# Performance work log

Measured on AMD Instinct MI355X. Metric: run time of the kernel, lower is better.

The kernel has to match this reference:

```python
import jax, jax.numpy as jnp
import numpy as np

N_NODES = 100000
N_EDGES = 1600000
N_GRAPHS = 512


def gcn_conv(x, row, col, W, b):
    # x: [N, Cin], row/col: [E] (self-loops already appended)
    n = x.shape[0]
    h = x @ W                                        # [N, Cout]
    deg = jax.ops.segment_sum(jnp.ones_like(col, dtype=x.dtype), col, num_segments=n)
    dinv = jnp.where(deg > 0, deg ** -0.5, 0.0)
    norm = dinv[row] * dinv[col]                     # [E]
    msg = norm[:, None] * h[row]                     # [E, Cout]
    out = jax.ops.segment_sum(msg, col, num_segments=n)
    return out + b


def setup_inputs() -> dict:
    key = jax.random.key(0)
    ks = jax.random.split(key, 10)
    x = jax.random.normal(ks[0], (N_NODES, 128), dtype=jnp.float32)
    edge_index = jax.random.randint(ks[1], (2, N_EDGES), 0, N_NODES, dtype=jnp.int64)
    batch = jnp.sort(jax.random.randint(ks[2], (N_NODES,), 0, N_GRAPHS, dtype=jnp.int64))
    def lin_w(k, fan_in, fan_out):
        bound = 1.0 / np.sqrt(fan_in)
        return jax.random.uniform(k, (fan_in, fan_out), jnp.float32, -bound, bound)
    # GCN layers (bias zero-initialized per reset_parameters)
    W1 = lin_w(ks[3], 128, 128); b1 = jnp.zeros((128,), jnp.float32)
    W2 = lin_w(ks[4], 128, 128); b2 = jnp.zeros((128,), jnp.float32)
    # MLP layers (Linear with bias)
    Wm1 = lin_w(ks[5], 128, 64)
    bm1 = jax.random.uniform(ks[6], (64,), jnp.float32, -1/np.sqrt(128), 1/np.sqrt(128))
    Wm2 = lin_w(ks[7], 64, 1)
    bm2 = jax.random.uniform(ks[8], (1,), jnp.float32, -1/np.sqrt(64), 1/np.sqrt(64))
    return {"x": x, "edge_index": edge_index, "batch": batch,
            "W1": W1, "b1": b1, "W2": W2, "b2": b2,
            "Wm1": Wm1, "bm1": bm1, "Wm2": Wm2, "bm2": bm2}


def reference(x, edge_index, batch, W1, b1, W2, b2, Wm1, bm1, Wm2, bm2):
    n = x.shape[0]
    loops = jnp.arange(n, dtype=edge_index.dtype)
    row = jnp.concatenate([edge_index[0], loops])
    col = jnp.concatenate([edge_index[1], loops])
    # GCN: conv -> relu -> conv
    h = gcn_conv(x, row, col, W1, b1)
    h = jax.nn.relu(h)
    h = gcn_conv(h, row, col, W2, b2)
    # scatter-mean pooling over graphs
    sums = jax.ops.segment_sum(h, batch, num_segments=N_GRAPHS)      # [G, C]
    counts = jax.ops.segment_sum(jnp.ones((n,), h.dtype), batch, num_segments=N_GRAPHS)
    g = sums / jnp.maximum(counts, 1.0)[:, None]
    # MLP: linear -> relu -> linear
    g = jax.nn.relu(g @ Wm1 + bm1)
    out = g @ Wm2 + bm2
    return out
```

## Files before the change

kernel.cpp:

```cpp
#include <hip/hip_runtime.h>
#include <math.h>

#define C_DIM 128
#define POOL_CHUNK 64
#define BKT_SHIFT 7
#define MAX_B 1024
#define CB 256
#define CHUNK_MAX 6400
#define FB_CAP 8192
typedef unsigned short ushort_t;
typedef __attribute__((ext_vector_type(8))) short short8;
typedef __attribute__((ext_vector_type(4))) float f32x4;

static inline int ceil_div(int a, int b) { return (a + b - 1) / b; }

__device__ inline ushort_t f2bf(float f) {
    union { float f; unsigned u; } v; v.f = f;
    unsigned r = v.u + 0x7FFFu + ((v.u >> 16) & 1u);
    return (ushort_t)(r >> 16);
}
__device__ inline float bf2f(unsigned s) {
    union { unsigned u; float f; } v; v.u = s << 16; return v.f;
}
__device__ inline float bf_lo(unsigned u) {
    union { unsigned v; float f; } c; c.v = u << 16; return c.f;
}
__device__ inline float bf_hi(unsigned u) {
    union { unsigned v; float f; } c; c.v = u & 0xFFFF0000u; return c.f;
}
__device__ inline void accum8(uint4 u, float acc[8]) {
    acc[0] += bf_lo(u.x); acc[1] += bf_hi(u.x);
    acc[2] += bf_lo(u.y); acc[3] += bf_hi(u.y);
    acc[4] += bf_lo(u.z); acc[5] += bf_hi(u.z);
    acc[6] += bf_lo(u.w); acc[7] += bf_hi(u.w);
}


__global__ __launch_bounds__(256) void k_sortchunk(
    const int* __restrict__ row, const int* __restrict__ col, int E, int chunk,
    int B, int* __restrict__ counts, int* __restrict__ sstart,
    int* __restrict__ epk,
    const float* __restrict__ W1, const float* __restrict__ W2,
    uint4* __restrict__ wf1, uint4* __restrict__ wf2,
    float* __restrict__ gsums, int GC, int* __restrict__ cursor) {
    int t = threadIdx.x, blk = blockIdx.x;
    if (blk >= CB) {
        const float* W = (blk == CB) ? W1 : W2;
        uint4* wf = (blk == CB) ? wf1 : wf2;
        for (int f = t; f < 2048; f += 256) {
            int lane = f & 63, kkn = f >> 6;
            int kk = kkn & 3, nt = kkn >> 2;
            int n = lane & 15, quad = lane >> 4;
            union { ushort_t h[8]; uint4 v; } u;
#pragma unroll
            for (int j = 0; j < 8; ++j)
                u.h[j] = f2bf(W[(size_t)(kk * 32 + quad * 8 + j) * C_DIM + nt * 16 + n]);
            wf[f] = u.v;
        }
        return;
    }
    for (int i = blk * 256 + t; i < GC; i += CB * 256) gsums[i] = 0.f;
    if (blk == 0 && t == 0) *cursor = 0;

    __shared__ int hist[MAX_B];
    __shared__ int hscan[MAX_B];
    __shared__ int sd[256];
    __shared__ int sorted[CHUNK_MAX];

    for (int i = t; i < B; i += 256) hist[i] = 0;
    __syncthreads();
    int s = blk * chunk;
    int e = s + chunk; if (e > E) e = E;
    for (int i = s + 4 * t; i < e; i += 1024) {
        int4 c = *(const int4*)(col + i);
        atomicAdd(&hist[c.x >> BKT_SHIFT], 1);
        atomicAdd(&hist[c.y >> BKT_SHIFT], 1);
        atomicAdd(&hist[c.z >> BKT_SHIFT], 1);
        atomicAdd(&hist[c.w >> BKT_SHIFT], 1);
    }
    __syncthreads();
    {
        int base4 = t * 4;
        int vv[4]; int sum = 0;
#pragma unroll
        for (int j = 0; j < 4; ++j) {
            int idx = base4 + j;
            vv[j] = (idx < B) ? hist[idx] : 0;
            sum += vv[j];
        }
        sd[t] = sum;
        __syncthreads();
        for (int off = 1; off < 256; off <<= 1) {
            int x = (t >= off) ? sd[t - off] : 0;
            __syncthreads();
            sd[t] += x;
            __syncthreads();
        }
        int run = sd[t] - sum;
#pragma unroll
        for (int j = 0; j < 4; ++j) {
            int idx = base4 + j;
            if (idx < B) hscan[idx] = run;
            run += vv[j];
        }
    }
    __syncthreads();
    for (int i = t; i < B; i += 256) {
        counts[(size_t)blk * MAX_B + i] = hist[i];
        sstart[(size_t)blk * MAX_B + i] = hscan[i];
    }
    __syncthreads();
    for (int i = t; i < B; i += 256) hist[i] = hscan[i];
    __syncthreads();
    for (int i = s + 4 * t; i < e; i += 1024) {
        int4 c = *(const int4*)(col + i);
        int4 r = *(const int4*)(row + i);
        int p0 = atomicAdd(&hist[c.x >> BKT_SHIFT], 1); sorted[p0] = (r.x << 7) | (c.x & 127);
        int p1 = atomicAdd(&hist[c.y >> BKT_SHIFT], 1); sorted[p1] = (r.y << 7) | (c.y & 127);
        int p2 = atomicAdd(&hist[c.z >> BKT_SHIFT], 1); sorted[p2] = (r.z << 7) | (c.z & 127);
        int p3 = atomicAdd(&hist[c.w >> BKT_SHIFT], 1); sorted[p3] = (r.w << 7) | (c.w & 127);
    }
    __syncthreads();
    int cnt = e - s;
    for (int i = t; i < cnt; i += 256) epk[s + i] = sorted[i];
}

__global__ __launch_bounds__(CB) void k_btotred(
    const int* __restrict__ counts, int* __restrict__ bbase,
    int* __restrict__ btot, int* __restrict__ cursor) {
    __shared__ int sd[CB];
    int b = blockIdx.x, t = threadIdx.x;
    sd[t] = counts[(size_t)t * MAX_B + b];
    __syncthreads();
    for (int off = CB / 2; off > 0; off >>= 1) {
        if (t < off) sd[t] += sd[t + off];
        __syncthreads();
    }
    if (t == 0) {
        int tot = sd[0];
        btot[b] = tot;
        bbase[b] = atomicAdd(cursor, tot);
    }
}

__global__ __launch_bounds__(256) void k_bfinal(
    const int* __restrict__ epk, const int* __restrict__ counts,
    const int* __restrict__ sstart, const int* __restrict__ bbase,
    const int* __restrict__ btot, int chunk, int N,
    int2* __restrict__ offs2, float* __restrict__ dinv, int* __restrict__ csr) {
    __shared__ int sh[FB_CAP];
    __shared__ int sd[256];
    __shared__ int cnt[128];
    __shared__ int pre[128];
    __shared__ int cur[128];
    int bkt = blockIdx.x, t = threadIdx.x;
    int sbase = bbase[bkt];
    int m = btot[bkt];
    int base = bkt << BKT_SHIFT;
    int nn = N - base; if (nn > 128) nn = 128;

    int segln = counts[(size_t)t * MAX_B + bkt];
    int gs = t * chunk + sstart[(size_t)t * MAX_B + bkt];
    sd[t] = segln;
    __syncthreads();
    for (int off = 1; off < 256; off <<= 1) {
        int x = (t >= off) ? sd[t - off] : 0;
        __syncthreads();
        sd[t] += x;
        __syncthreads();
    }
    int place = sd[t] - segln;

    bool fits = (m <= FB_CAP);
    if (t < 128) cnt[t] = 0;
    __syncthreads();
    if (fits) {
        for (int j = 0; j < segln; ++j) {
            int u = epk[gs + j];
            sh[place + j] = u;
            atomicAdd(&cnt[u & 127], 1);
        }
    } else {
        for (int j = 0; j < segln; ++j)
            atomicAdd(&cnt[epk[gs + j] & 127], 1);
    }
    __syncthreads();
    if (t < 128) pre[t] = cnt[t];
    __syncthreads();
    for (int off = 1; off < 128; off <<= 1) {
        int x = (t >= off && t < 128) ? pre[t - off] : 0;
        __syncthreads();
        if (t < 128) pre[t] += x;
        __syncthreads();
    }
    if (t < 128) {
        int ex = pre[t] - cnt[t];
        cur[t] = ex;
        if (t < nn) {
            offs2[base + t] = make_int2(sbase + ex, sbase + ex + cnt[t]);
            dinv[base + t] = 1.0f / sqrtf((float)cnt[t] + 1.0f);
        }
    }
    __syncthreads();
    if (fits) {
        for (int i = t; i < m; i += 256) {
            int u = sh[i];
            int slot = atomicAdd(&cur[u & 127], 1);
            csr[sbase + slot] = u >> 7;
        }
    } else {
        for (int j = 0; j < segln; ++j) {
            int u = epk[gs + j];
            int slot = atomicAdd(&cur[u & 127], 1);
            csr[sbase + slot] = u >> 7;
        }
    }
}

template <int ABF16>
__global__ __launch_bounds__(256) void k_matmul_mfma(
    const float* __restrict__ Af, const ushort_t* __restrict__ Abf,
    const uint4* __restrict__ wfrag, const float* __restrict__ dinv,
    ushort_t* __restrict__ Cb, int N) {
    __shared__ uint4 wfs[2048];
    __shared__ __align__(16) ushort_t As[64 * 136];
    int t = threadIdx.x;
    int wv = t >> 6, lane = t & 63;
    int n = lane & 15, quad = lane >> 4;
    int row0 = blockIdx.x * 64;

    for (int i = t; i < 2048; i += 256) wfs[i] = wfrag[i];

    if (ABF16) {
#pragma unroll
        for (int i = 0; i < 4; ++i) {
            int idx = i * 256 + t;
            int r = idx >> 4, c8 = idx & 15;
            int grow = row0 + r; if (grow >= N) grow = N - 1;
            uint4 u = *(const uint4*)(Abf + (size_t)grow * C_DIM + c8 * 8);
            *(uint4*)&As[r * 136 + c8 * 8] = u;
        }
    } else {
#pragma unroll
        for (int i = 0; i < 8; ++i) {
            int idx = i * 256 + t;
            int r = idx >> 5, cq = idx & 31;
            int grow = row0 + r; if (grow >= N) grow = N - 1;
            float4 f = *(const float4*)(Af + (size_t)grow * C_DIM + cq * 4);
            union { ushort_t h[4]; uint2 v; } c;
            c.h[0] = f2bf(f.x); c.h[1] = f2bf(f.y);
            c.h[2] = f2bf(f.z); c.h[3] = f2bf(f.w);
            *(uint2*)&As[r * 136 + cq * 4] = c.v;
        }
    }

    f32x4 acc[8];
#pragma unroll
    for (int i = 0; i < 8; ++i) acc[i] = (f32x4){0.f, 0.f, 0.f, 0.f};

    __syncthreads();

    int rl = wv * 16 + n;
#pragma unroll
    for (int kk = 0; kk < 4; ++kk) {
        union { uint4 v; short8 s; } ca;
        ca.v = *(const uint4*)&As[rl * 136 + kk * 32 + quad * 8];
#pragma unroll
        for (int nt = 0; nt < 8; ++nt) {
            union { uint4 v; short8 s; } cb;
            cb.v = wfs[(nt * 4 + kk) * 64 + lane];
            acc[nt] = __builtin_amdgcn_mfma_f32_16x16x32_bf16(ca.s, cb.s, acc[nt], 0, 0, 0);
        }
    }

    __syncthreads();
#pragma unroll
    for (int reg = 0; reg < 4; ++reg) {
        int lr = wv * 16 + quad * 4 + reg;
        int grow = row0 + lr;
        float sc = dinv[grow < N ? grow : N - 1];
#pragma unroll
        for (int nt = 0; nt < 8; ++nt)
            As[lr * 136 + nt * 16 + n] = f2bf(acc[nt][reg] * sc);
    }
    __syncthreads();
    int rows = N - row0; if (rows > 64) rows = 64;
    for (int idx = t; idx < 16 * 64; idx += 256) {
        int r = idx >> 4, c8 = idx & 15;
        if (r < rows)
            *(uint4*)(Cb + (size_t)(row0 + r) * C_DIM + c8 * 8) =
                *(const uint4*)&As[r * 136 + c8 * 8];
    }
}

template <int RELU>
__global__ __launch_bounds__(256) void k_aggregate(
    const ushort_t* __restrict__ hs, const int2* __restrict__ offs2,
    const int* __restrict__ csr, const float* __restrict__ dinv,
    const float* __restrict__ bias, uint4* __restrict__ outV, int N) {
    int node = (blockIdx.x << 2) + (threadIdx.x >> 6);
    if (node >= N) return;
    int t = threadIdx.x & 63;
    int q = t >> 4;
    int fs = t & 15;
    int2 se = offs2[node];
    int s = se.x, e = se.y;

    float acc[8];
    {
        uint4 u = *(const uint4*)(hs + (size_t)node * C_DIM + fs * 8);
        float v[8];
        v[0] = bf_lo(u.x); v[1] = bf_hi(u.x);
        v[2] = bf_lo(u.y); v[3] = bf_hi(u.y);
        v[4] = bf_lo(u.z); v[5] = bf_hi(u.z);
        v[6] = bf_lo(u.w); v[7] = bf_hi(u.w);
#pragma unroll
        for (int i = 0; i < 8; ++i) acc[i] = (q == 0) ? v[i] : 0.f;
    }

    int j = s;
    for (; j + 16 <= e; j += 16) {
        int r[4];
#pragma unroll
        for (int b = 0; b < 4; ++b) r[b] = csr[j + b * 4 + q];
        uint4 u[4];
#pragma unroll
        for (int b = 0; b < 4; ++b)
            u[b] = *(const uint4*)(hs + (size_t)r[b] * C_DIM + fs * 8);
#pragma unroll
        for (int b = 0; b < 4; ++b) accum8(u[b], acc);
    }
    for (; j + 4 <= e; j += 4) {
        int r = csr[j + q];
        uint4 u = *(const uint4*)(hs + (size_t)r * C_DIM + fs * 8);
        accum8(u, acc);
    }
    if (j + q < e) {
        int r = csr[j + q];
        uint4 u = *(const uint4*)(hs + (size_t)r * C_DIM + fs * 8);
        accum8(u, acc);
    }

#pragma unroll
    for (int i = 0; i < 8; ++i) {
        acc[i] += __shfl_xor(acc[i], 16);
        acc[i] += __shfl_xor(acc[i], 32);
    }

    if (q == 0) {
        float dn = dinv[node];
        float4 b0 = *(const float4*)(bias + fs * 8);
        float4 b1 = *(const float4*)(bias + fs * 8 + 4);
        float o[8];
        o[0] = dn * acc[0] + b0.x; o[1] = dn * acc[1] + b0.y;
        o[2] = dn * acc[2] + b0.z; o[3] = dn * acc[3] + b0.w;
        o[4] = dn * acc[4] + b1.x; o[5] = dn * acc[5] + b1.y;
        o[6] = dn * acc[6] + b1.z; o[7] = dn * acc[7] + b1.w;
        if (RELU) {
#pragma unroll
            for (int i = 0; i < 8; ++i) o[i] = fmaxf(o[i], 0.f);
        }
        uint4 pk;
        pk.x = (unsigned)f2bf(o[0]) | ((unsigned)f2bf(o[1]) << 16);
        pk.y = (unsigned)f2bf(o[2]) | ((unsigned)f2bf(o[3]) << 16);
        pk.z = (unsigned)f2bf(o[4]) | ((unsigned)f2bf(o[5]) << 16);
        pk.w = (unsigned)f2bf(o[6]) | ((unsigned)f2bf(o[7]) << 16);
        outV[(size_t)node * 16 + fs] = pk;
    }
}

__global__ __launch_bounds__(128) void k_pool_sum(
    const ushort_t* __restrict__ h, const int* __restrict__ batch, int n,
    float* __restrict__ sums) {
    int r0 = blockIdx.x * POOL_CHUNK;
    int r1 = r0 + POOL_CHUNK; if (r1 > n) r1 = n;
    if (r0 >= n) return;
    int t = threadIdx.x;
    int c = t & 63, rr = t >> 6;
    float2 acc = make_float2(0.f, 0.f);
    int g = batch[r0];
    int i = r0;
    while (i < r1) {
        if (i + 8 <= r1 && batch[i + 7] == g) {
#pragma unroll
            for (int b = 0; b < 4; ++b) {
                unsigned u = *(const unsigned*)(h + (size_t)(i + rr + 2 * b) * C_DIM + c * 2);
                acc.x += bf_lo(u); acc.y += bf_hi(u);
            }
            i += 8;
        } else {
            int bi = batch[i];
            if (bi != g) {
                atomicAdd(&sums[(size_t)g * C_DIM + c * 2], acc.x);
                atomicAdd(&sums[(size_t)g * C_DIM + c * 2 + 1], acc.y);
                acc = make_float2(0.f, 0.f); g = bi;
            }
            if (rr == 0) {
                unsigned u = *(const unsigned*)(h + (size_t)i * C_DIM + c * 2);
                acc.x += bf_lo(u); acc.y += bf_hi(u);
            }
            ++i;
        }
    }
    atomicAdd(&sums[(size_t)g * C_DIM + c * 2], acc.x);
    atomicAdd(&sums[(size_t)g * C_DIM + c * 2 + 1], acc.y);
}

__global__ __launch_bounds__(128) void k_mlp(
    const float* __restrict__ sums, const int* __restrict__ batch, int n,
    const float* __restrict__ Wm1, const float* __restrict__ bm1,
    const float* __restrict__ Wm2, const float* __restrict__ bm2,
    float* __restrict__ out) {
    int g = blockIdx.x;
    int t = threadIdx.x;
    int lo = 0, hi = n;
    while (lo < hi) { int m = (lo + hi) >> 1; if (batch[m] < g) lo = m + 1; else hi = m; }
    int start = lo;
    lo = start; hi = n;
    while (lo < hi) { int m = (lo + hi) >> 1; if (batch[m] < g + 1) lo = m + 1; else hi = m; }
    float cnt = (float)(lo - start);

    float mean = sums[(size_t)g * C_DIM + t] / fmaxf(cnt, 1.0f);

    __shared__ float m_s[128];
    __shared__ float hid[64];
    m_s[t] = mean;
    __syncthreads();
    if (t < 64) {
        float a = bm1[t];
#pragma unroll 4
        for (int k = 0; k < 128; ++k) a += m_s[k] * Wm1[k * 64 + t];
        hid[t] = fmaxf(a, 0.f) * Wm2[t];
    }
    __syncthreads();
    if (t < 64) {
        float v = hid[t];
        for (int off = 32; off > 0; off >>= 1) v += __shfl_down(v, off);
        if (t == 0) out[g] = v + bm2[0];
    }
}

extern "C" void kernel_launch(void* const* d_in, const int* in_sizes, int n_in,
                              void* d_out, int out_size, void* d_ws, size_t ws_size,
                              hipStream_t stream) {
    const float* x     = (const float*)d_in[0];
    const int*   eidx  = (const int*)d_in[1];
    const int*   batch = (const int*)d_in[2];
    const float* W1    = (const float*)d_in[3];
    const float* b1    = (const float*)d_in[4];
    const float* W2    = (const float*)d_in[5];
    const float* b2    = (const float*)d_in[6];
    const float* Wm1   = (const float*)d_in[7];
    const float* bm1   = (const float*)d_in[8];
    const float* Wm2   = (const float*)d_in[9];
    const float* bm2   = (const float*)d_in[10];

    const int N = in_sizes[2];
    const int E = in_sizes[1] / 2;
    const int G = out_size;
    const int B = (N + 127) >> BKT_SHIFT;

    char* p = (char*)d_ws;
    auto carve = [&](size_t bytes) {
        char* q = p;
        p += (bytes + 255) & ~(size_t)255;
        return q;
    };
    ushort_t* bufT   = (ushort_t*)carve((size_t)N * C_DIM * sizeof(ushort_t));
    ushort_t* bufA   = (ushort_t*)carve((size_t)N * C_DIM * sizeof(ushort_t));
    float*    dinv   = (float*)   carve((size_t)N * sizeof(float));
    int2*     offs2  = (int2*)    carve((size_t)N * sizeof(int2));
    int*      csr    = (int*)     carve((size_t)E * sizeof(int));
    int*      counts = (int*)     carve((size_t)CB * MAX_B * sizeof(int));
    int*      sstart = (int*)     carve((size_t)CB * MAX_B * sizeof(int));
    int*      btot   = (int*)     carve((size_t)B * sizeof(int));
    int*      bbase  = (int*)     carve((size_t)B * sizeof(int));
    float*    gsums  = (float*)   carve((size_t)G * C_DIM * sizeof(float));
    uint4*    wf1    = (uint4*)   carve(2048 * sizeof(uint4));
    uint4*    wf2    = (uint4*)   carve(2048 * sizeof(uint4));
    int*      cursor = (int*)     carve(sizeof(int));
    int*      epk    = (int*)bufT;

    const int* erow = eidx;
    const int* ecol = eidx + E;
    const int chunk = (ceil_div(E, CB) + 3) & ~3;

    k_sortchunk<<<CB + 2, 256, 0, stream>>>(erow, ecol, E, chunk, B,
                                            counts, sstart, epk,
                                            W1, W2, wf1, wf2, gsums, G * C_DIM, cursor);
    k_btotred<<<B, CB, 0, stream>>>(counts, bbase, btot, cursor);
    k_bfinal<<<B, 256, 0, stream>>>(epk, counts, sstart, bbase, btot, chunk, N,
                                    offs2, dinv, csr);

    k_matmul_mfma<0><<<ceil_div(N, 64), 256, 0, stream>>>(x, nullptr, wf1, dinv, bufT, N);
    k_aggregate<1><<<ceil_div(N, 4), 256, 0, stream>>>(bufT, offs2, csr, dinv, b1,
                                                       (uint4*)bufA, N);
    k_matmul_mfma<1><<<ceil_div(N, 64), 256, 0, stream>>>(nullptr, bufA, wf2, dinv, bufT, N);
    k_aggregate<0><<<ceil_div(N, 4), 256, 0, stream>>>(bufT, offs2, csr, dinv, b2,
                                                       (uint4*)bufA, N);
    k_pool_sum<<<ceil_div(N, POOL_CHUNK), 128, 0, stream>>>(bufA, batch, N, gsums);
    k_mlp<<<G, 128, 0, stream>>>(gsums, batch, N, Wm1, bm1, Wm2, bm2, (float*)d_out);
}
```

Baseline: 318.5 us.

## Stage edges in LDS for sort, fold bucket-total kernel, enlarge matmul tile

The chunk sort now loads row/col once, packs edges and bucket ids into shared memory during the histogram pass, and scatters from LDS instead of re-reading global memory. It also writes the sorted chunk out with vectorized stores. The separate bucket-total reduction kernel is removed: k_bfinal takes the total from its own prefix scan and claims its base offset with an atomic on the cursor, saving one launch. The MFMA matmul now handles 128 rows per block with two accumulator tiles per wave, reusing each weight fragment twice. The costs are more LDS per block (about 51 KB extra in the sort, 34 KB in the matmul), more registers, and fewer matmul blocks in flight.

```diff
diff --git a/kernel.cpp b/kernel.cpp
--- a/kernel.cpp
+++ b/kernel.cpp
@@ -65,18 +65,35 @@
     __shared__ int hist[MAX_B];
     __shared__ int hscan[MAX_B];
     __shared__ int sd[256];
+    __shared__ __align__(16) int ebuf[CHUNK_MAX];
+    __shared__ __align__(8)  ushort_t bbuf[CHUNK_MAX];
     __shared__ int sorted[CHUNK_MAX];
 
     for (int i = t; i < B; i += 256) hist[i] = 0;
     __syncthreads();
     int s = blk * chunk;
     int e = s + chunk; if (e > E) e = E;
+    int cnt = e - s;
     for (int i = s + 4 * t; i < e; i += 1024) {
         int4 c = *(const int4*)(col + i);
-        atomicAdd(&hist[c.x >> BKT_SHIFT], 1);
-        atomicAdd(&hist[c.y >> BKT_SHIFT], 1);
-        atomicAdd(&hist[c.z >> BKT_SHIFT], 1);
-        atomicAdd(&hist[c.w >> BKT_SHIFT], 1);
+        int4 r = *(const int4*)(row + i);
+        int li = i - s;
+        int4 pk;
+        pk.x = (r.x << 7) | (c.x & 127);
+        pk.y = (r.y << 7) | (c.y & 127);
+        pk.z = (r.z << 7) | (c.z & 127);
+        pk.w = (r.w << 7) | (c.w & 127);
+        *(int4*)&ebuf[li] = pk;
+        ushort4 bk;
+        bk.x = (ushort_t)(c.x >> BKT_SHIFT);
+        bk.y = (ushort_t)(c.y >> BKT_SHIFT);
+        bk.z = (ushort_t)(c.z >> BKT_SHIFT);
+        bk.w = (ushort_t)(c.w >> BKT_SHIFT);
+        *(ushort4*)&bbuf[li] = bk;
+        atomicAdd(&hist[bk.x], 1);
+        atomicAdd(&hist[bk.y], 1);
+        atomicAdd(&hist[bk.z], 1);
+        atomicAdd(&hist[bk.w], 1);
     }
     __syncthreads();
     {
@@ -112,50 +129,27 @@
     __syncthreads();
     for (int i = t; i < B; i += 256) hist[i] = hscan[i];
     __syncthreads();
-    for (int i = s + 4 * t; i < e; i += 1024) {
-        int4 c = *(const int4*)(col + i);
-        int4 r = *(const int4*)(row + i);
-        int p0 = atomicAdd(&hist[c.x >> BKT_SHIFT], 1); sorted[p0] = (r.x << 7) | (c.x & 127);
-        int p1 = atomicAdd(&hist[c.y >> BKT_SHIFT], 1); sorted[p1] = (r.y << 7) | (c.y & 127);
-        int p2 = atomicAdd(&hist[c.z >> BKT_SHIFT], 1); sorted[p2] = (r.z << 7) | (c.z & 127);
-        int p3 = atomicAdd(&hist[c.w >> BKT_SHIFT], 1); sorted[p3] = (r.w << 7) | (c.w & 127);
-    }
-    __syncthreads();
-    int cnt = e - s;
-    for (int i = t; i < cnt; i += 256) epk[s + i] = sorted[i];
-}
-
-__global__ __launch_bounds__(CB) void k_btotred(
-    const int* __restrict__ counts, int* __restrict__ bbase,
-    int* __restrict__ btot, int* __restrict__ cursor) {
-    __shared__ int sd[CB];
-    int b = blockIdx.x, t = threadIdx.x;
-    sd[t] = counts[(size_t)t * MAX_B + b];
-    __syncthreads();
-    for (int off = CB / 2; off > 0; off >>= 1) {
-        if (t < off) sd[t] += sd[t + off];
-        __syncthreads();
-    }
-    if (t == 0) {
-        int tot = sd[0];
-        btot[b] = tot;
-        bbase[b] = atomicAdd(cursor, tot);
-    }
+    for (int i = t; i < cnt; i += 256) {
+        int pos = atomicAdd(&hist[bbuf[i]], 1);
+        sorted[pos] = ebuf[i];
+    }
+    __syncthreads();
+    for (int i = t; i * 4 < cnt; i += 256)
+        *(int4*)&epk[s + i * 4] = *(const int4*)&sorted[i * 4];
 }
 
 __global__ __launch_bounds__(256) void k_bfinal(
     const int* __restrict__ epk, const int* __restrict__ counts,
-    const int* __restrict__ sstart, const int* __restrict__ bbase,
-    const int* __restrict__ btot, int chunk, int N,
+    const int* __restrict__ sstart, int* __restrict__ cursor,
+    int chunk, int N,
     int2* __restrict__ offs2, float* __restrict__ dinv, int* __restrict__ csr) {
     __shared__ int sh[FB_CAP];
     __shared__ int sd[256];
     __shared__ int cnt[128];
     __shared__ int pre[128];
     __shared__ int cur[128];
+    __shared__ int sbase_s;
     int bkt = blockIdx.x, t = threadIdx.x;
-    int sbase = bbase[bkt];
-    int m = btot[bkt];
     int base = bkt << BKT_SHIFT;
     int nn = N - base; if (nn > 128) nn = 128;
 
@@ -170,10 +164,13 @@
         __syncthreads();
     }
     int place = sd[t] - segln;
+    int m = sd[255];
+    if (t == 255) sbase_s = atomicAdd(cursor, m);
+    if (t < 128) cnt[t] = 0;
+    __syncthreads();
+    int sbase = sbase_s;
 
     bool fits = (m <= FB_CAP);
-    if (t < 128) cnt[t] = 0;
-    __syncthreads();
     if (fits) {
         for (int j = 0; j < segln; ++j) {
             int u = epk[gs + j];
@@ -223,17 +220,17 @@
     const uint4* __restrict__ wfrag, const float* __restrict__ dinv,
     ushort_t* __restrict__ Cb, int N) {
     __shared__ uint4 wfs[2048];
-    __shared__ __align__(16) ushort_t As[64 * 136];
+    __shared__ __align__(16) ushort_t As[128 * 136];
     int t = threadIdx.x;
     int wv = t >> 6, lane = t & 63;
     int n = lane & 15, quad = lane >> 4;
-    int row0 = blockIdx.x * 64;
+    int row0 = blockIdx.x * 128;
 
     for (int i = t; i < 2048; i += 256) wfs[i] = wfrag[i];
 
     if (ABF16) {
 #pragma unroll
-        for (int i = 0; i < 4; ++i) {
+        for (int i = 0; i < 8; ++i) {
             int idx = i * 256 + t;
             int r = idx >> 4, c8 = idx & 15;
             int grow = row0 + r; if (grow >= N) grow = N - 1;
@@ -242,7 +239,7 @@
         }
     } else {
 #pragma unroll
-        for (int i = 0; i < 8; ++i) {
+        for (int i = 0; i < 16; ++i) {
             int idx = i * 256 + t;
             int r = idx >> 5, cq = idx & 31;
             int grow = row0 + r; if (grow >= N) grow = N - 1;
@@ -254,38 +251,47 @@
         }
     }
 
-    f32x4 acc[8];
-#pragma unroll
-    for (int i = 0; i < 8; ++i) acc[i] = (f32x4){0.f, 0.f, 0.f, 0.f};
-
-    __syncthreads();
-
-    int rl = wv * 16 + n;
+    f32x4 acc[2][8];
+#pragma unroll
+    for (int tl = 0; tl < 2; ++tl)
+#pragma unroll
+        for (int i = 0; i < 8; ++i) acc[tl][i] = (f32x4){0.f, 0.f, 0.f, 0.f};
+
+    __syncthreads();
+
+    int rl0 = wv * 32 + n;
+    int rl1 = rl0 + 16;
 #pragma unroll
     for (int kk = 0; kk < 4; ++kk) {
-        union { uint4 v; short8 s; } ca;
-        ca.v = *(const uint4*)&As[rl * 136 + kk * 32 + quad * 8];
+        union { uint4 v; short8 s; } ca0, ca1;
+        ca0.v = *(const uint4*)&As[rl0 * 136 + kk * 32 + quad * 8];
+        ca1.v = *(const uint4*)&As[rl1 * 136 + kk * 32 + quad * 8];
 #pragma unroll
         for (int nt = 0; nt < 8; ++nt) {
             union { uint4 v; short8 s; } cb;
             cb.v = wfs[(nt * 4 + kk) * 64 + lane];
-            acc[nt] = __builtin_amdgcn_mfma_f32_16x16x32_bf16(ca.s, cb.s, acc[nt], 0, 0, 0);
-        }
-    }
-
-    __syncthreads();
+            acc[0][nt] = __builtin_amdgcn_mfma_f32_16x16x32_bf16(ca0.s, cb.s, acc[0][nt], 0, 0, 0);
+            acc[1][nt] = __builtin_amdgcn_mfma_f32_16x16x32_bf16(ca1.s, cb.s, acc[1][nt], 0, 0, 0);
+        }
+    }
+
+    __syncthreads();
+#pragma unroll
+    for (int tl = 0; tl < 2; ++tl)
 #pragma unroll
     for (int reg = 0; reg < 4; ++reg) {
-        int lr = wv * 16 + quad * 4 + reg;
+        int lr = wv * 32 + tl * 16 + quad * 4 + reg;
         int grow = row0 + lr;
         float sc = dinv[grow < N ? grow : N - 1];
 #pragma unroll
         for (int nt = 0; nt < 8; ++nt)
-            As[lr * 136 + nt * 16 + n] = f2bf(acc[nt][reg] * sc);
-    }
-    __syncthreads();
-    int rows = N - row0; if (rows > 64) rows = 64;
-    for (int idx = t; idx < 16 * 64; idx += 256) {
+            As[lr * 136 + nt * 16 + n] = f2bf(acc[tl][nt][reg] * sc);
+    }
+    __syncthreads();
+    int rows = N - row0; if (rows > 128) rows = 128;
+#pragma unroll
+    for (int i = 0; i < 8; ++i) {
+        int idx = i * 256 + t;
         int r = idx >> 4, c8 = idx & 15;
         if (r < rows)
             *(uint4*)(Cb + (size_t)(row0 + r) * C_DIM + c8 * 8) =
@@ -473,8 +479,6 @@
     int*      csr    = (int*)     carve((size_t)E * sizeof(int));
     int*      counts = (int*)     carve((size_t)CB * MAX_B * sizeof(int));
     int*      sstart = (int*)     carve((size_t)CB * MAX_B * sizeof(int));
-    int*      btot   = (int*)     carve((size_t)B * sizeof(int));
-    int*      bbase  = (int*)     carve((size_t)B * sizeof(int));
     float*    gsums  = (float*)   carve((size_t)G * C_DIM * sizeof(float));
     uint4*    wf1    = (uint4*)   carve(2048 * sizeof(uint4));
     uint4*    wf2    = (uint4*)   carve(2048 * sizeof(uint4));
@@ -488,14 +492,13 @@
     k_sortchunk<<<CB + 2, 256, 0, stream>>>(erow, ecol, E, chunk, B,
                                             counts, sstart, epk,
                                             W1, W2, wf1, wf2, gsums, G * C_DIM, cursor);
-    k_btotred<<<B, CB, 0, stream>>>(counts, bbase, btot, cursor);
-    k_bfinal<<<B, 256, 0, stream>>>(epk, counts, sstart, bbase, btot, chunk, N,
+    k_bfinal<<<B, 256, 0, stream>>>(epk, counts, sstart, cursor, chunk, N,
                                     offs2, dinv, csr);
 
-    k_matmul_mfma<0><<<ceil_div(N, 64), 256, 0, stream>>>(x, nullptr, wf1, dinv, bufT, N);
+    k_matmul_mfma<0><<<ceil_div(N, 128), 256, 0, stream>>>(x, nullptr, wf1, dinv, bufT, N);
     k_aggregate<1><<<ceil_div(N, 4), 256, 0, stream>>>(bufT, offs2, csr, dinv, b1,
                                                        (uint4*)bufA, N);
-    k_matmul_mfma<1><<<ceil_div(N, 64), 256, 0, stream>>>(nullptr, bufA, wf2, dinv, bufT, N);
+    k_matmul_mfma<1><<<ceil_div(N, 128), 256, 0, stream>>>(nullptr, bufA, wf2, dinv, bufT, N);
     k_aggregate<0><<<ceil_div(N, 4), 256, 0, stream>>>(bufT, offs2, csr, dinv, b2,
                                                        (uint4*)bufA, N);
     k_pool_sum<<<ceil_div(N, POOL_CHUNK), 128, 0, stream>>>(bufA, batch, N, gsums);
```

Measured after the change: 318.4 us. Within noise of the previous version (-0.0%).
